# Kernel optimization log

Measured on AMD Instinct MI355X. Metric: run time of the kernel, lower is better.

The kernel has to match this reference:

```python
import jax, jax.numpy as jnp
import numpy as np

N_LEAVES = 16384
D = 1024
L = 32


def _build_full_binary_tree(n_leaves):
    # Leaves are node ids [0, n_leaves); internal nodes are assigned ids level by
    # level bottom-up, so children always have smaller ids than their parent and
    # left_idx/right_idx are grouped contiguously per level.
    level_nodes = np.arange(n_leaves)
    nid = n_leaves
    lefts, rights = [], []
    while level_nodes.size > 1:
        lefts.append(level_nodes[0::2])
        rights.append(level_nodes[1::2])
        w = level_nodes.size // 2
        level_nodes = np.arange(nid, nid + w)
        nid += w
    return np.concatenate(lefts).astype(np.int32), np.concatenate(rights).astype(np.int32)


def setup_inputs() -> dict:
    key = jax.random.key(0)
    k_h, k_t, k_w = jax.random.split(key, 3)
    n_nodes = 2 * N_LEAVES - 1
    hidden = jax.random.normal(k_h, (n_nodes, D), dtype=jnp.float32)
    # xavier_normal-ish scales
    trans = jax.random.normal(k_t, (L, L), dtype=jnp.float32) * (2.0 / (L + L)) ** 0.5
    W_pred = jax.random.normal(k_w, (L, 2 * D), dtype=jnp.float32) * (2.0 / (2 * D + L)) ** 0.5
    b_pred = jnp.zeros((L,), dtype=jnp.float32)
    left_idx, right_idx = _build_full_binary_tree(N_LEAVES)
    return {
        "hidden": hidden,
        "trans": trans,
        "W_pred": W_pred,
        "b_pred": b_pred,
        "left_idx": jnp.asarray(left_idx),
        "right_idx": jnp.asarray(right_idx),
    }


def reference(hidden, trans, W_pred, b_pred, left_idx, right_idx):
    # hidden: [N, D] node bottom-up hidden states; N = 2*n_leaves - 1
    n_nodes, d = hidden.shape
    n_leaves = (n_nodes + 1) // 2
    num_labels = trans.shape[0]

    # collect_avg_hidden: mean over all node hidden states
    avg_h = jnp.mean(hidden, axis=0)  # [D]
    # avg_h_pred: emission = Linear(concat(h, avg_h))  -> [N, L]
    feats = jnp.concatenate(
        [hidden, jnp.broadcast_to(avg_h, hidden.shape)], axis=1
    )  # [N, 2D]
    emission = feats @ W_pred.T + b_pred  # [N, L]

    # Inside DP, bottom-up, batched by tree level. For an internal node p:
    #   inside[p, y] = logsumexp_{l,r}( emission[p,y] + trans[y,l] + inside_left[l]
    #                                   + trans[y,r] + inside_right[r] )
    # which factorizes exactly into two independent logsumexps.
    scores = jnp.zeros((n_nodes, num_labels), dtype=hidden.dtype)
    scores = scores.at[:n_leaves].set(emission[:n_leaves])

    pos = 0
    node_base = n_leaves
    width = n_leaves // 2
    while width >= 1:  # fixed log2(n_leaves) structural levels
        li = left_idx[pos:pos + width]
        ri = right_idx[pos:pos + width]
        ls = scores[li]  # [width, L]
        rs = scores[ri]  # [width, L]
        # trans[y, c] + child_score[c], logsumexp over child label c
        left_m = jax.nn.logsumexp(trans[None, :, :] + ls[:, None, :], axis=2)
        right_m = jax.nn.logsumexp(trans[None, :, :] + rs[:, None, :], axis=2)
        new = emission[node_base:node_base + width] + left_m + right_m
        scores = scores.at[node_base:node_base + width].set(new)
        pos += width
        node_base += width
        width //= 2

    return scores[n_nodes - 1]  # root inside score, [L]
```

## Files before the change

kernel.cpp:

```cpp
#include <hip/hip_runtime.h>

#define NN 32767
#define NL 16384
#define DD 1024
#define LL 32

typedef __attribute__((ext_vector_type(8))) short bf16x8;
typedef __attribute__((ext_vector_type(4))) float f32x4;

__device__ __forceinline__ short f2bf(float f) {
  union { float f; unsigned u; } x; x.f = f;
  unsigned r = x.u + 0x7FFFu + ((x.u >> 16) & 1u);
  return (short)(r >> 16);
}

__device__ __forceinline__ bf16x8 cvt8(float4 a, float4 b) {
  bf16x8 r;
  r[0] = f2bf(a.x); r[1] = f2bf(a.y); r[2] = f2bf(a.z); r[3] = f2bf(a.w);
  r[4] = f2bf(b.x); r[5] = f2bf(b.y); r[6] = f2bf(b.z); r[7] = f2bf(b.w);
  return r;
}

__global__ __launch_bounds__(256) void pack_kernel(const float* __restrict__ Wp,
                                                   short* __restrict__ Wpk) {
  int idx = blockIdx.x * 256 + threadIdx.x;
  #pragma unroll
  for (int t = 0; t < 4; ++t, idx += 16384) {
    const int j = idx & 7, m = (idx >> 3) & 3, lane = (idx >> 5) & 63, s = idx >> 11;
    const int wrow = (lane & 15) + 16 * (m & 1);
    const int wcol = (m >> 1) * 1024 + s * 32 + (lane >> 4) * 8 + j;
    Wpk[idx] = f2bf(Wp[(size_t)wrow * (2 * DD) + wcol]);
  }
}

__global__ __launch_bounds__(1024, 4) void gemm_kernel(
    const float* __restrict__ hidden, const short* __restrict__ Wpk,
    float* __restrict__ E0, float* __restrict__ gpartB) {
  __shared__ float cmb[8 * 1024];
  __shared__ float part2[8][LL];
  const int tid = threadIdx.x;
  const int wid = tid >> 6, lane = tid & 63;
  const int wt = wid & 7, kh = wid >> 3;
  const int tile = blockIdx.x * 8 + wt;
  const int mrow = lane & 15, g = lane >> 4;
  int grow = tile * 16 + mrow;
  if (grow > NN - 1) grow = NN - 1;

  const float*  ap = hidden + (size_t)grow * DD + kh * 512 + g * 8;
  const bf16x8* wb = (const bf16x8*)Wpk + kh * 4096 + lane * 4;

  f32x4 acc0 = {0,0,0,0}, acc1 = {0,0,0,0}, acc2 = {0,0,0,0}, acc3 = {0,0,0,0};

  #pragma unroll
  for (int c = 0; c < 8; ++c) {
    float4 a0 = *(const float4*)(ap + c * 64);
    float4 a1 = *(const float4*)(ap + c * 64 + 4);
    float4 a2 = *(const float4*)(ap + c * 64 + 32);
    float4 a3 = *(const float4*)(ap + c * 64 + 36);
    const bf16x8* p = wb + c * 512;
    bf16x8 w0 = p[0],   w1 = p[1],   w2 = p[2],   w3 = p[3];
    bf16x8 x0 = p[256], x1 = p[257], x2 = p[258], x3 = p[259];
    bf16x8 af0 = cvt8(a0, a1);
    acc0 = __builtin_amdgcn_mfma_f32_16x16x32_bf16(af0, w0, acc0, 0, 0, 0);
    acc1 = __builtin_amdgcn_mfma_f32_16x16x32_bf16(af0, w1, acc1, 0, 0, 0);
    acc2 = __builtin_amdgcn_mfma_f32_16x16x32_bf16(af0, w2, acc2, 0, 0, 0);
    acc3 = __builtin_amdgcn_mfma_f32_16x16x32_bf16(af0, w3, acc3, 0, 0, 0);
    bf16x8 af1 = cvt8(a2, a3);
    acc0 = __builtin_amdgcn_mfma_f32_16x16x32_bf16(af1, x0, acc0, 0, 0, 0);
    acc1 = __builtin_amdgcn_mfma_f32_16x16x32_bf16(af1, x1, acc1, 0, 0, 0);
    acc2 = __builtin_amdgcn_mfma_f32_16x16x32_bf16(af1, x2, acc2, 0, 0, 0);
    acc3 = __builtin_amdgcn_mfma_f32_16x16x32_bf16(af1, x3, acc3, 0, 0, 0);
  }

  float* cl = cmb + wt * 1024 + lane * 16;
  if (kh == 1) {
    *(f32x4*)(cl)      = acc0;
    *(f32x4*)(cl + 4)  = acc1;
    *(f32x4*)(cl + 8)  = acc2;
    *(f32x4*)(cl + 12) = acc3;
  }
  __syncthreads();
  if (kh == 0) {
    acc0 += *(const f32x4*)(cl);
    acc1 += *(const f32x4*)(cl + 4);
    acc2 += *(const f32x4*)(cl + 8);
    acc3 += *(const f32x4*)(cl + 12);
    #pragma unroll
    for (int r = 0; r < 4; ++r) {
      const int srow = tile * 16 + g * 4 + r;
      if (srow < NN) {
        E0[(size_t)srow * LL + mrow]      = acc0[r];
        E0[(size_t)srow * LL + mrow + 16] = acc1[r];
      }
    }
    if (tile == 2047 && g == 3) { acc2[3] = 0.f; acc3[3] = 0.f; }
    float s2 = acc2[0] + acc2[1] + acc2[2] + acc2[3];
    float s3 = acc3[0] + acc3[1] + acc3[2] + acc3[3];
    s2 += __shfl_xor(s2, 16, 64); s2 += __shfl_xor(s2, 32, 64);
    s3 += __shfl_xor(s3, 16, 64); s3 += __shfl_xor(s3, 32, 64);
    if (lane < 32) part2[wt][lane] = (lane < 16) ? s2 : s3;
  }
  __syncthreads();
  if (tid < LL) {
    float s = 0.f;
    #pragma unroll
    for (int q = 0; q < 8; ++q) s += part2[q][tid];
    gpartB[blockIdx.x * LL + tid] = s;
  }
}

__device__ __forceinline__ float lse32(const float4* tt, const float4* sv) {
  float m = -3.0e38f;
  float4 v[8];
  #pragma unroll
  for (int i = 0; i < 8; ++i) {
    float4 t = tt[i], s = sv[i], w;
    w.x = t.x + s.x; w.y = t.y + s.y; w.z = t.z + s.z; w.w = t.w + s.w;
    v[i] = w;
    m = fmaxf(m, fmaxf(fmaxf(w.x, w.y), fmaxf(w.z, w.w)));
  }
  float ss = 0.f;
  #pragma unroll
  for (int i = 0; i < 8; ++i) {
    ss += __expf(v[i].x - m) + __expf(v[i].y - m) +
          __expf(v[i].z - m) + __expf(v[i].w - m);
  }
  return m + __logf(ss);
}

__device__ __forceinline__ void compute_cvec(const float* __restrict__ gpartB,
                                             const float* __restrict__ bp,
                                             float* cv, float (*pr)[LL]) {
  const int tid = threadIdx.x;
  const int j = tid & 31, r = tid >> 5;
  float s = 0.f;
  #pragma unroll
  for (int q = 0; q < 8; ++q) s += gpartB[(size_t)(r + q * 32) * LL + j];
  pr[r][j] = s;
  __syncthreads();
  if (tid < LL) {
    float ss = 0.f;
    #pragma unroll
    for (int q = 0; q < 32; ++q) ss += pr[q][tid];
    cv[tid] = bp[tid] + ss * (1.0f / (float)NN);
  }
  __syncthreads();
}

__global__ __launch_bounds__(1024) void tree_kernel(
    const float* __restrict__ E0, const float* __restrict__ gpartB,
    const float* __restrict__ bp, const float* __restrict__ trans,
    const float* __restrict__ src, float* __restrict__ dst,
    int base1, int leafmode) {
  __shared__ __align__(16) float cv[LL];
  __shared__ float pr[32][LL];
  __shared__ float l1[16][LL], l2[8][LL], l3[4][LL];
  compute_cvec(gpartB, bp, cv, pr);

  const int wid = threadIdx.x >> 6, lane = threadIdx.x & 63;
  const int j = lane & 31, half = lane >> 5;
  const int b = blockIdx.x, G = gridDim.x;
  float4 tt[8];
  #pragma unroll
  for (int i = 0; i < 8; ++i) tt[i] = *(const float4*)(trans + j * LL + i * 4);
  const float cj = cv[j];
  float4 sv[8];

  {
    const int n = b * 16 + wid;
    const float* sp = src + (size_t)(2 * n + half) * LL;
    if (leafmode) {
      #pragma unroll
      for (int i = 0; i < 8; ++i) {
        float4 vv = *(const float4*)(sp + i * 4);
        float4 c4 = *(const float4*)(cv + i * 4);
        vv.x += c4.x; vv.y += c4.y; vv.z += c4.z; vv.w += c4.w;
        sv[i] = vv;
      }
    } else {
      #pragma unroll
      for (int i = 0; i < 8; ++i) sv[i] = *(const float4*)(sp + i * 4);
    }
    float lsum = lse32(tt, sv);
    float other = __shfl_xor(lsum, 32, 64);
    float o = E0[(size_t)(base1 + n) * LL + j] + cj + lsum + other;
    if (lane < 32) l1[wid][j] = o;
  }
  __syncthreads();
  const int base2 = base1 + G * 16;
  if (wid < 8) {
    const float* sp = l1[2 * wid + half];
    #pragma unroll
    for (int i = 0; i < 8; ++i) sv[i] = *(const float4*)(sp + i * 4);
    float lsum = lse32(tt, sv);
    float other = __shfl_xor(lsum, 32, 64);
    float o = E0[(size_t)(base2 + b * 8 + wid) * LL + j] + cj + lsum + other;
    if (lane < 32) l2[wid][j] = o;
  }
  __syncthreads();
  const int base3 = base2 + G * 8;
  if (wid < 4) {
    const float* sp = l2[2 * wid + half];
    #pragma unroll
    for (int i = 0; i < 8; ++i) sv[i] = *(const float4*)(sp + i * 4);
    float lsum = lse32(tt, sv);
    float other = __shfl_xor(lsum, 32, 64);
    float o = E0[(size_t)(base3 + b * 4 + wid) * LL + j] + cj + lsum + other;
    if (lane < 32) l3[wid][j] = o;
  }
  __syncthreads();
  const int base4 = base3 + G * 4;
  if (wid < 2) {
    const float* sp = l3[2 * wid + half];
    #pragma unroll
    for (int i = 0; i < 8; ++i) sv[i] = *(const float4*)(sp + i * 4);
    float lsum = lse32(tt, sv);
    float other = __shfl_xor(lsum, 32, 64);
    float o = E0[(size_t)(base4 + b * 2 + wid) * LL + j] + cj + lsum + other;
    if (lane < 32) l1[wid][j] = o;
  }
  __syncthreads();
  const int base5 = base4 + G * 2;
  if (wid == 0) {
    const float* sp = l1[half];
    #pragma unroll
    for (int i = 0; i < 8; ++i) sv[i] = *(const float4*)(sp + i * 4);
    float lsum = lse32(tt, sv);
    float other = __shfl_xor(lsum, 32, 64);
    float o = E0[(size_t)(base5 + b) * LL + j] + cj + lsum + other;
    if (lane < 32) dst[(size_t)b * LL + j] = o;
  }
}

__global__ __launch_bounds__(1024) void tail_kernel(
    const float* __restrict__ E0, const float* __restrict__ gpartB,
    const float* __restrict__ bp, const float* __restrict__ trans,
    const float* __restrict__ S10, float* __restrict__ out) {
  __shared__ __align__(16) float cv[LL];
  __shared__ float pr[32][LL];
  __shared__ float t1[8][LL], t2[4][LL], t3[2][LL];
  compute_cvec(gpartB, bp, cv, pr);

  const int wid = threadIdx.x >> 6, lane = threadIdx.x & 63;
  const int j = lane & 31, half = lane >> 5;
  float4 tt[8];
  #pragma unroll
  for (int i = 0; i < 8; ++i) tt[i] = *(const float4*)(trans + j * LL + i * 4);
  const float cj = cv[j];
  float4 sv[8];

  if (wid < 8) {
    const float* sp = S10 + (size_t)(2 * wid + half) * LL;
    #pragma unroll
    for (int i = 0; i < 8; ++i) sv[i] = *(const float4*)(sp + i * 4);
    float lsum = lse32(tt, sv);
    float other = __shfl_xor(lsum, 32, 64);
    float o = E0[(size_t)(32752 + wid) * LL + j] + cj + lsum + other;
    if (lane < 32) t1[wid][j] = o;
  }
  __syncthreads();
  if (wid < 4) {
    const float* sp = t1[2 * wid + half];
    #pragma unroll
    for (int i = 0; i < 8; ++i) sv[i] = *(const float4*)(sp + i * 4);
    float lsum = lse32(tt, sv);
    float other = __shfl_xor(lsum, 32, 64);
    float o = E0[(size_t)(32760 + wid) * LL + j] + cj + lsum + other;
    if (lane < 32) t2[wid][j] = o;
  }
  __syncthreads();
  if (wid < 2) {
    const float* sp = t2[2 * wid + half];
    #pragma unroll
    for (int i = 0; i < 8; ++i) sv[i] = *(const float4*)(sp + i * 4);
    float lsum = lse32(tt, sv);
    float other = __shfl_xor(lsum, 32, 64);
    float o = E0[(size_t)(32764 + wid) * LL + j] + cj + lsum + other;
    if (lane < 32) t3[wid][j] = o;
  }
  __syncthreads();
  if (wid == 0) {
    const float* sp = t3[half];
    #pragma unroll
    for (int i = 0; i < 8; ++i) sv[i] = *(const float4*)(sp + i * 4);
    float lsum = lse32(tt, sv);
    float other = __shfl_xor(lsum, 32, 64);
    float o = E0[(size_t)32766 * LL + j] + cj + lsum + other;
    if (lane < 32) out[j] = o;
  }
}

extern "C" void kernel_launch(void* const* d_in, const int* in_sizes, int n_in,
                              void* d_out, int out_size, void* d_ws, size_t ws_size,
                              hipStream_t stream) {
  const float* hidden = (const float*)d_in[0];
  const float* trans  = (const float*)d_in[1];
  const float* Wp     = (const float*)d_in[2];
  const float* bp     = (const float*)d_in[3];

  float* ws     = (float*)d_ws;
  float* E0     = ws;
  float* gpartB = E0 + (size_t)NN * LL;
  float* S5     = gpartB + 256 * LL;
  float* S10    = S5 + 512 * LL;
  short* Wpk    = (short*)(S10 + 16 * LL);

  pack_kernel<<<64, 256, 0, stream>>>(Wp, Wpk);
  gemm_kernel<<<256, 1024, 0, stream>>>(hidden, Wpk, E0, gpartB);
  tree_kernel<<<512, 1024, 0, stream>>>(E0, gpartB, bp, trans, E0, S5, 16384, 1);
  tree_kernel<<<16, 1024, 0, stream>>>(E0, gpartB, bp, trans, S5, S10, 32256, 0);
  tail_kernel<<<1, 1024, 0, stream>>>(E0, gpartB, bp, trans, S10, (float*)d_out);
}
```

Before: 81.77 us.

## Double-buffer GEMM via async global-to-LDS loads and merge upper tree levels into tail

Restructures the emission GEMM as 512 blocks of 256 threads. Each block stages its hidden-row and weight chunks into swizzled LDS double buffers with global_load_lds, and overlaps the next chunk's loads with the current chunk's MFMA work. This replaces the earlier split-K direct-load scheme. The second tree launch is removed, and the single-block tail kernel now walks all remaining levels from width 256 down to the root using a large LDS scratch. That saves one launch but puts more serial work in a single block.

New measurement: 115.0 us. +40.7%, slower.

```diff
diff --git a/kernel.cpp b/kernel.cpp
--- a/kernel.cpp
+++ b/kernel.cpp
@@ -7,6 +7,8 @@
 
 typedef __attribute__((ext_vector_type(8))) short bf16x8;
 typedef __attribute__((ext_vector_type(4))) float f32x4;
+
+#define MFMA __builtin_amdgcn_mfma_f32_16x16x32_bf16
 
 __device__ __forceinline__ short f2bf(float f) {
   union { float f; unsigned u; } x; x.f = f;
@@ -21,6 +23,12 @@
   return r;
 }
 
+__device__ __forceinline__ void gld_lds16(const float* g, float* l) {
+  __builtin_amdgcn_global_load_lds(
+      (const __attribute__((address_space(1))) void*)g,
+      (__attribute__((address_space(3))) void*)l, 16, 0, 0);
+}
+
 __global__ __launch_bounds__(256) void pack_kernel(const float* __restrict__ Wp,
                                                    short* __restrict__ Wpk) {
   int idx = blockIdx.x * 256 + threadIdx.x;
@@ -33,79 +41,118 @@
   }
 }
 
-__global__ __launch_bounds__(1024, 4) void gemm_kernel(
+__global__ __launch_bounds__(256, 2) void gemm_kernel(
     const float* __restrict__ hidden, const short* __restrict__ Wpk,
     float* __restrict__ E0, float* __restrict__ gpartB) {
-  __shared__ float cmb[8 * 1024];
-  __shared__ float part2[8][LL];
+  __shared__ float Abuf[2][4096];
+  __shared__ float Wbuf[2][2048];
+  __shared__ float part2[4][LL];
+
   const int tid = threadIdx.x;
-  const int wid = tid >> 6, lane = tid & 63;
-  const int wt = wid & 7, kh = wid >> 3;
-  const int tile = blockIdx.x * 8 + wt;
+  const int w = tid >> 6, lane = tid & 63;
   const int mrow = lane & 15, g = lane >> 4;
-  int grow = tile * 16 + mrow;
-  if (grow > NN - 1) grow = NN - 1;
-
-  const float*  ap = hidden + (size_t)grow * DD + kh * 512 + g * 8;
-  const bf16x8* wb = (const bf16x8*)Wpk + kh * 4096 + lane * 4;
+  const int b = blockIdx.x;
+
+  const float* pA0; const float* pA1; const float* pA2; const float* pA3;
+  #define MKA(R_, P_) { const int U = (R_)*256 + tid;                        \
+    const int lr = U >> 4, u = U & 15;                                       \
+    int grow = b * 64 + lr; if (grow > NN - 1) grow = NN - 1;                \
+    P_ = hidden + (size_t)grow * DD + ((u ^ (lr & 7)) << 2); }
+  MKA(0, pA0) MKA(1, pA1) MKA(2, pA2) MKA(3, pA3)
+  #undef MKA
+  const short* pW = Wpk + lane * 32 + w * 8;
+
+  const int aoff0 = 0 * 1024 + w * 256;
+  const int aoff1 = 1 * 1024 + w * 256;
+  const int aoff2 = 2 * 1024 + w * 256;
+  const int aoff3 = 3 * 1024 + w * 256;
+  const int woff0 = w * 256;
+  const int woff1 = 1024 + w * 256;
+
+  const int r7 = mrow & 7;
+  const int rowb = (w * 16 + mrow) * 64;
+  const int lane4 = lane * 4;
+  const int au00 = ((2 * g) ^ r7) << 2;
+  const int au01 = ((2 * g + 1) ^ r7) << 2;
+  const int au10 = ((8 + 2 * g) ^ r7) << 2;
+  const int au11 = ((9 + 2 * g) ^ r7) << 2;
 
   f32x4 acc0 = {0,0,0,0}, acc1 = {0,0,0,0}, acc2 = {0,0,0,0}, acc3 = {0,0,0,0};
 
-  #pragma unroll
-  for (int c = 0; c < 8; ++c) {
-    float4 a0 = *(const float4*)(ap + c * 64);
-    float4 a1 = *(const float4*)(ap + c * 64 + 4);
-    float4 a2 = *(const float4*)(ap + c * 64 + 32);
-    float4 a3 = *(const float4*)(ap + c * 64 + 36);
-    const bf16x8* p = wb + c * 512;
-    bf16x8 w0 = p[0],   w1 = p[1],   w2 = p[2],   w3 = p[3];
-    bf16x8 x0 = p[256], x1 = p[257], x2 = p[258], x3 = p[259];
-    bf16x8 af0 = cvt8(a0, a1);
-    acc0 = __builtin_amdgcn_mfma_f32_16x16x32_bf16(af0, w0, acc0, 0, 0, 0);
-    acc1 = __builtin_amdgcn_mfma_f32_16x16x32_bf16(af0, w1, acc1, 0, 0, 0);
-    acc2 = __builtin_amdgcn_mfma_f32_16x16x32_bf16(af0, w2, acc2, 0, 0, 0);
-    acc3 = __builtin_amdgcn_mfma_f32_16x16x32_bf16(af0, w3, acc3, 0, 0, 0);
-    bf16x8 af1 = cvt8(a2, a3);
-    acc0 = __builtin_amdgcn_mfma_f32_16x16x32_bf16(af1, x0, acc0, 0, 0, 0);
-    acc1 = __builtin_amdgcn_mfma_f32_16x16x32_bf16(af1, x1, acc1, 0, 0, 0);
-    acc2 = __builtin_amdgcn_mfma_f32_16x16x32_bf16(af1, x2, acc2, 0, 0, 0);
-    acc3 = __builtin_amdgcn_mfma_f32_16x16x32_bf16(af1, x3, acc3, 0, 0, 0);
-  }
-
-  float* cl = cmb + wt * 1024 + lane * 16;
-  if (kh == 1) {
-    *(f32x4*)(cl)      = acc0;
-    *(f32x4*)(cl + 4)  = acc1;
-    *(f32x4*)(cl + 8)  = acc2;
-    *(f32x4*)(cl + 12) = acc3;
-  }
-  __syncthreads();
-  if (kh == 0) {
-    acc0 += *(const f32x4*)(cl);
-    acc1 += *(const f32x4*)(cl + 4);
-    acc2 += *(const f32x4*)(cl + 8);
-    acc3 += *(const f32x4*)(cl + 12);
-    #pragma unroll
-    for (int r = 0; r < 4; ++r) {
-      const int srow = tile * 16 + g * 4 + r;
-      if (srow < NN) {
-        E0[(size_t)srow * LL + mrow]      = acc0[r];
-        E0[(size_t)srow * LL + mrow + 16] = acc1[r];
-      }
+#define STAGE(KC) {                                                          \
+    float* ab_ = Abuf[(KC) & 1];                                             \
+    gld_lds16(pA0 + (KC) * 64, ab_ + aoff0);                                 \
+    gld_lds16(pA1 + (KC) * 64, ab_ + aoff1);                                 \
+    gld_lds16(pA2 + (KC) * 64, ab_ + aoff2);                                 \
+    gld_lds16(pA3 + (KC) * 64, ab_ + aoff3);                                 \
+    float* wb_ = Wbuf[(KC) & 1];                                             \
+    gld_lds16((const float*)(pW + (size_t)(KC) * 4096),        wb_ + woff0); \
+    gld_lds16((const float*)(pW + (size_t)(KC) * 4096 + 2048), wb_ + woff1); }
+
+#define COMPUTE(KC) {                                                        \
+    const float* ab_ = Abuf[(KC) & 1] + rowb;                                \
+    const float* wb_ = Wbuf[(KC) & 1];                                       \
+    float4 a0 = *(const float4*)(ab_ + au00);                                \
+    float4 a1 = *(const float4*)(ab_ + au01);                                \
+    bf16x8 af0 = cvt8(a0, a1);                                               \
+    bf16x8 w0 = *(const bf16x8*)(wb_ + lane4);                               \
+    bf16x8 w1 = *(const bf16x8*)(wb_ + 256 + lane4);                         \
+    bf16x8 w2 = *(const bf16x8*)(wb_ + 512 + lane4);                         \
+    bf16x8 w3 = *(const bf16x8*)(wb_ + 768 + lane4);                         \
+    acc0 = MFMA(af0, w0, acc0, 0,0,0);                                       \
+    acc1 = MFMA(af0, w1, acc1, 0,0,0);                                       \
+    acc2 = MFMA(af0, w2, acc2, 0,0,0);                                       \
+    acc3 = MFMA(af0, w3, acc3, 0,0,0);                                       \
+    float4 a2 = *(const float4*)(ab_ + au10);                                \
+    float4 a3 = *(const float4*)(ab_ + au11);                                \
+    bf16x8 af1 = cvt8(a2, a3);                                               \
+    bf16x8 x0 = *(const bf16x8*)(wb_ + 1024 + lane4);                        \
+    bf16x8 x1 = *(const bf16x8*)(wb_ + 1280 + lane4);                        \
+    bf16x8 x2 = *(const bf16x8*)(wb_ + 1536 + lane4);                        \
+    bf16x8 x3 = *(const bf16x8*)(wb_ + 1792 + lane4);                        \
+    acc0 = MFMA(af1, x0, acc0, 0,0,0);                                       \
+    acc1 = MFMA(af1, x1, acc1, 0,0,0);                                       \
+    acc2 = MFMA(af1, x2, acc2, 0,0,0);                                       \
+    acc3 = MFMA(af1, x3, acc3, 0,0,0); }
+
+#define CHUNK(KC) {                                                          \
+    STAGE(KC + 1)                                                            \
+    asm volatile("s_waitcnt vmcnt(6)" ::: "memory");                         \
+    __builtin_amdgcn_s_barrier();                                            \
+    COMPUTE(KC)                                                              \
+    __builtin_amdgcn_s_barrier(); }
+
+  STAGE(0)
+  CHUNK(0)  CHUNK(1)  CHUNK(2)  CHUNK(3)
+  CHUNK(4)  CHUNK(5)  CHUNK(6)  CHUNK(7)
+  CHUNK(8)  CHUNK(9)  CHUNK(10) CHUNK(11)
+  CHUNK(12) CHUNK(13) CHUNK(14)
+  asm volatile("s_waitcnt vmcnt(0)" ::: "memory");
+  __builtin_amdgcn_s_barrier();
+  COMPUTE(15)
+#undef CHUNK
+#undef COMPUTE
+#undef STAGE
+
+  #pragma unroll
+  for (int r = 0; r < 4; ++r) {
+    const int srow = b * 64 + w * 16 + g * 4 + r;
+    if (srow < NN) {
+      E0[(size_t)srow * LL + mrow]      = acc0[r];
+      E0[(size_t)srow * LL + mrow + 16] = acc1[r];
     }
-    if (tile == 2047 && g == 3) { acc2[3] = 0.f; acc3[3] = 0.f; }
-    float s2 = acc2[0] + acc2[1] + acc2[2] + acc2[3];
-    float s3 = acc3[0] + acc3[1] + acc3[2] + acc3[3];
-    s2 += __shfl_xor(s2, 16, 64); s2 += __shfl_xor(s2, 32, 64);
-    s3 += __shfl_xor(s3, 16, 64); s3 += __shfl_xor(s3, 32, 64);
-    if (lane < 32) part2[wt][lane] = (lane < 16) ? s2 : s3;
-  }
+  }
+  const int tile = b * 4 + w;
+  if (tile == 2047 && g == 3) { acc2[3] = 0.f; acc3[3] = 0.f; }
+  float s2 = acc2[0] + acc2[1] + acc2[2] + acc2[3];
+  float s3 = acc3[0] + acc3[1] + acc3[2] + acc3[3];
+  s2 += __shfl_xor(s2, 16, 64); s2 += __shfl_xor(s2, 32, 64);
+  s3 += __shfl_xor(s3, 16, 64); s3 += __shfl_xor(s3, 32, 64);
+  if (lane < 32) part2[w][lane] = (lane < 16) ? s2 : s3;
   __syncthreads();
   if (tid < LL) {
-    float s = 0.f;
-    #pragma unroll
-    for (int q = 0; q < 8; ++q) s += part2[q][tid];
-    gpartB[blockIdx.x * LL + tid] = s;
+    float s = part2[0][tid] + part2[1][tid] + part2[2][tid] + part2[3][tid];
+    gpartB[b * LL + tid] = s;
   }
 }
 
@@ -135,7 +182,7 @@
   const int j = tid & 31, r = tid >> 5;
   float s = 0.f;
   #pragma unroll
-  for (int q = 0; q < 8; ++q) s += gpartB[(size_t)(r + q * 32) * LL + j];
+  for (int q = 0; q < 16; ++q) s += gpartB[(size_t)(r + q * 32) * LL + j];
   pr[r][j] = s;
   __syncthreads();
   if (tid < LL) {
@@ -150,8 +197,7 @@
 __global__ __launch_bounds__(1024) void tree_kernel(
     const float* __restrict__ E0, const float* __restrict__ gpartB,
     const float* __restrict__ bp, const float* __restrict__ trans,
-    const float* __restrict__ src, float* __restrict__ dst,
-    int base1, int leafmode) {
+    float* __restrict__ dst) {
   __shared__ __align__(16) float cv[LL];
   __shared__ float pr[32][LL];
   __shared__ float l1[16][LL], l2[8][LL], l3[4][LL];
@@ -165,21 +211,17 @@
   for (int i = 0; i < 8; ++i) tt[i] = *(const float4*)(trans + j * LL + i * 4);
   const float cj = cv[j];
   float4 sv[8];
+  const int base1 = NL;
 
   {
     const int n = b * 16 + wid;
-    const float* sp = src + (size_t)(2 * n + half) * LL;
-    if (leafmode) {
-      #pragma unroll
-      for (int i = 0; i < 8; ++i) {
-        float4 vv = *(const float4*)(sp + i * 4);
-        float4 c4 = *(const float4*)(cv + i * 4);
-        vv.x += c4.x; vv.y += c4.y; vv.z += c4.z; vv.w += c4.w;
-        sv[i] = vv;
-      }
-    } else {
-      #pragma unroll
-      for (int i = 0; i < 8; ++i) sv[i] = *(const float4*)(sp + i * 4);
+    const float* sp = E0 + (size_t)(2 * n + half) * LL;
+    #pragma unroll
+    for (int i = 0; i < 8; ++i) {
+      float4 vv = *(const float4*)(sp + i * 4);
+      float4 c4 = *(const float4*)(cv + i * 4);
+      vv.x += c4.x; vv.y += c4.y; vv.z += c4.z; vv.w += c4.w;
+      sv[i] = vv;
     }
     float lsum = lse32(tt, sv);
     float other = __shfl_xor(lsum, 32, 64);
@@ -235,10 +277,10 @@
 __global__ __launch_bounds__(1024) void tail_kernel(
     const float* __restrict__ E0, const float* __restrict__ gpartB,
     const float* __restrict__ bp, const float* __restrict__ trans,
-    const float* __restrict__ S10, float* __restrict__ out) {
+    const float* __restrict__ S5, float* __restrict__ out) {
   __shared__ __align__(16) float cv[LL];
   __shared__ float pr[32][LL];
-  __shared__ float t1[8][LL], t2[4][LL], t3[2][LL];
+  __shared__ float ts[511 * LL];
   compute_cvec(gpartB, bp, cv, pr);
 
   const int wid = threadIdx.x >> 6, lane = threadIdx.x & 63;
@@ -249,44 +291,27 @@
   const float cj = cv[j];
   float4 sv[8];
 
-  if (wid < 8) {
-    const float* sp = S10 + (size_t)(2 * wid + half) * LL;
-    #pragma unroll
-    for (int i = 0; i < 8; ++i) sv[i] = *(const float4*)(sp + i * 4);
-    float lsum = lse32(tt, sv);
-    float other = __shfl_xor(lsum, 32, 64);
-    float o = E0[(size_t)(32752 + wid) * LL + j] + cj + lsum + other;
-    if (lane < 32) t1[wid][j] = o;
-  }
-  __syncthreads();
-  if (wid < 4) {
-    const float* sp = t1[2 * wid + half];
-    #pragma unroll
-    for (int i = 0; i < 8; ++i) sv[i] = *(const float4*)(sp + i * 4);
-    float lsum = lse32(tt, sv);
-    float other = __shfl_xor(lsum, 32, 64);
-    float o = E0[(size_t)(32760 + wid) * LL + j] + cj + lsum + other;
-    if (lane < 32) t2[wid][j] = o;
-  }
-  __syncthreads();
-  if (wid < 2) {
-    const float* sp = t2[2 * wid + half];
-    #pragma unroll
-    for (int i = 0; i < 8; ++i) sv[i] = *(const float4*)(sp + i * 4);
-    float lsum = lse32(tt, sv);
-    float other = __shfl_xor(lsum, 32, 64);
-    float o = E0[(size_t)(32764 + wid) * LL + j] + cj + lsum + other;
-    if (lane < 32) t3[wid][j] = o;
-  }
-  __syncthreads();
-  if (wid == 0) {
-    const float* sp = t3[half];
-    #pragma unroll
-    for (int i = 0; i < 8; ++i) sv[i] = *(const float4*)(sp + i * 4);
-    float lsum = lse32(tt, sv);
-    float other = __shfl_xor(lsum, 32, 64);
-    float o = E0[(size_t)32766 * LL + j] + cj + lsum + other;
-    if (lane < 32) out[j] = o;
+  int width = 256, pnode = 32256, cIdxBase = -1;
+  while (width >= 1) {
+    for (int n = wid; n < width; n += 16) {
+      const float* sp = (cIdxBase < 0)
+          ? (S5 + (size_t)(2 * n + half) * LL)
+          : (ts + (size_t)(cIdxBase + 2 * n + half) * LL);
+      #pragma unroll
+      for (int i = 0; i < 8; ++i) sv[i] = *(const float4*)(sp + i * 4);
+      float lsum = lse32(tt, sv);
+      float other = __shfl_xor(lsum, 32, 64);
+      if (lane < 32) {
+        const int node = pnode + n;
+        float o = E0[(size_t)node * LL + j] + cj + lsum + other;
+        ts[(size_t)(node - 32256) * LL + j] = o;
+        if (node == NN - 1) out[j] = o;
+      }
+    }
+    __syncthreads();
+    cIdxBase = pnode - 32256;
+    pnode += width;
+    width >>= 1;
   }
 }
 
@@ -301,13 +326,11 @@
   float* ws     = (float*)d_ws;
   float* E0     = ws;
   float* gpartB = E0 + (size_t)NN * LL;
-  float* S5     = gpartB + 256 * LL;
-  float* S10    = S5 + 512 * LL;
-  short* Wpk    = (short*)(S10 + 16 * LL);
+  float* S5     = gpartB + 512 * LL;
+  short* Wpk    = (short*)(S5 + 512 * LL);
 
   pack_kernel<<<64, 256, 0, stream>>>(Wp, Wpk);
-  gemm_kernel<<<256, 1024, 0, stream>>>(hidden, Wpk, E0, gpartB);
-  tree_kernel<<<512, 1024, 0, stream>>>(E0, gpartB, bp, trans, E0, S5, 16384, 1);
-  tree_kernel<<<16, 1024, 0, stream>>>(E0, gpartB, bp, trans, S5, S10, 32256, 0);
-  tail_kernel<<<1, 1024, 0, stream>>>(E0, gpartB, bp, trans, S10, (float*)d_out);
-}
+  gemm_kernel<<<512, 256, 0, stream>>>(hidden, Wpk, E0, gpartB);
+  tree_kernel<<<512, 1024, 0, stream>>>(E0, gpartB, bp, trans, S5);
+  tail_kernel<<<1, 1024, 0, stream>>>(E0, gpartB, bp, trans, S5, (float*)d_out);
+}
```
